# Kernel optimization log

Measured on AMD Instinct MI355X. Metric: run time of the kernel, lower is better.

## Reference

```python
import jax, jax.numpy as jnp
import numpy as np

B, T, D = 16, 2048, 384
BLOCK = 3
NB = D // BLOCK
EPS = 1e-8


def setup_inputs() -> dict:
    key = jax.random.key(0)
    ks = jax.random.split(key, 8)
    std = 0.02
    quat_sequence = jax.random.normal(ks[0], (B, T, 4), dtype=jnp.float32)
    # weights stored as (in, out); x @ W
    W_in = jax.random.normal(ks[1], (4, D), dtype=jnp.float32) * std
    W_biv = jax.random.normal(ks[2], (D, NB * 3), dtype=jnp.float32) * (1.0 / np.sqrt(D))
    b_biv = jnp.zeros((NB * 3,), dtype=jnp.float32)
    W_dec = jax.random.normal(ks[3], (D, D), dtype=jnp.float32) * (1.0 / np.sqrt(D))
    b_dec = jnp.full((D,), 1.4, dtype=jnp.float32)
    W_inj = jax.random.normal(ks[4], (D, D), dtype=jnp.float32) * (1.0 / np.sqrt(D))
    b_inj = jax.random.normal(ks[5], (D,), dtype=jnp.float32) * (1.0 / np.sqrt(D))
    W_out = jax.random.normal(ks[6], (D, 4), dtype=jnp.float32) * std
    return {
        'quat_sequence': quat_sequence,
        'W_in': W_in, 'W_biv': W_biv, 'b_biv': b_biv,
        'W_dec': W_dec, 'b_dec': b_dec, 'W_inj': W_inj, 'b_inj': b_inj,
        'W_out': W_out,
    }


def _quat_rotate_blocks(h_blocks, bivectors):
    # h_blocks, bivectors: (..., NB, 3)
    norm_b = jnp.clip(jnp.linalg.norm(bivectors, axis=-1, keepdims=True), EPS, None)
    half = norm_b / 2
    w = jnp.cos(half)[..., 0]
    s = (jnp.sin(half) / norm_b)[..., 0]
    qx = s * bivectors[..., 2]
    qy = -s * bivectors[..., 1]
    qz = s * bivectors[..., 0]
    vx, vy, vz = h_blocks[..., 0], h_blocks[..., 1], h_blocks[..., 2]
    tx = 2 * (qy * vz - qz * vy)
    ty = 2 * (qz * vx - qx * vz)
    tz = 2 * (qx * vy - qy * vx)
    rx = vx + w * tx + (qy * tz - qz * ty)
    ry = vy + w * ty + (qz * tx - qx * tz)
    rz = vz + w * tz + (qx * ty - qy * tx)
    return jnp.stack([rx, ry, rz], axis=-1)


def reference(quat_sequence, W_in, W_biv, b_biv, W_dec, b_dec, W_inj, b_inj, W_out):
    hidden_input = quat_sequence @ W_in                       # (B,T,D)
    bivectors_all = (hidden_input @ W_biv + b_biv).reshape(B, T, NB, 3)
    decay_all = jax.nn.sigmoid(hidden_input @ W_dec + b_dec)  # (B,T,D)
    injection_all = hidden_input @ W_inj + b_inj              # (B,T,D)

    def step(h, xs):
        biv, dec, inj = xs  # (B,NB,3), (B,D), (B,D)
        rot = _quat_rotate_blocks(h.reshape(B, NB, 3), biv).reshape(B, D)
        h_next = dec * rot + inj
        return h_next, h_next

    h0 = jnp.zeros((B, D), dtype=quat_sequence.dtype)
    xs = (jnp.swapaxes(bivectors_all, 0, 1),
          jnp.swapaxes(decay_all, 0, 1),
          jnp.swapaxes(injection_all, 0, 1))
    _, hidden_seq = jax.lax.scan(step, h0, xs)                # (T,B,D)
    hidden_output = jnp.swapaxes(hidden_seq, 0, 1)            # (B,T,D)

    predicted_raw = hidden_output @ W_out                     # (B,T,4)
    norm = jnp.clip(jnp.linalg.norm(predicted_raw, axis=-1, keepdims=True), EPS, None)
    return predicted_raw / norm
```

## Files before the change

kernel.cpp:

```cpp
#include <hip/hip_runtime.h>
#include <hip/hip_bf16.h>

#define BB 16
#define TT 2048
#define DD 384
#define GG 2048
#define CC 256
#define LL 8
#define HSTRIDE (DD + 8)
#define EPSF 1e-8f
#define RCPF(x) __builtin_amdgcn_rcpf(x)

__global__ __launch_bounds__(256) void precompute_wc(
        const float* __restrict__ W_in,
        const float* __restrict__ W_biv,
        const float* __restrict__ W_dec,
        const float* __restrict__ W_inj,
        float* __restrict__ Wc) {
    int m = blockIdx.x;
    int jl = threadIdx.x & 15;
    int dp = threadIdx.x >> 4;
    int j = blockIdx.y * 16 + jl;
    const float* __restrict__ W = (m == 0) ? W_biv : (m == 1) ? W_dec : W_inj;
    float a[4] = {0.f, 0.f, 0.f, 0.f};
    for (int d = dp; d < DD; d += 16) {
        float wv = W[d * DD + j];
#pragma unroll
        for (int k = 0; k < 4; ++k) a[k] = fmaf(W_in[k * DD + d], wv, a[k]);
    }
    __shared__ float red[16][17][4];
#pragma unroll
    for (int k = 0; k < 4; ++k) red[dp][jl][k] = a[k];
    __syncthreads();
    for (int s = 8; s >= 1; s >>= 1) {
        if (dp < s) {
#pragma unroll
            for (int k = 0; k < 4; ++k) red[dp][jl][k] += red[dp + s][jl][k];
        }
        __syncthreads();
    }
    if (dp < 4)
        Wc[(size_t)m * 4 * DD + dp * DD + j] = red[0][jl][dp];
}

struct Wts {
    float wb[4][3], wd[4][3], wi[4][3];
    float bb[3], bd[3], bj[3];
};

__device__ __forceinline__ void load_wts(const float* __restrict__ Wc,
                                         const float* __restrict__ b_biv,
                                         const float* __restrict__ b_dec,
                                         const float* __restrict__ b_inj,
                                         int j0, Wts& W) {
    const float* __restrict__ Wb = Wc;
    const float* __restrict__ Wd = Wc + 4 * DD;
    const float* __restrict__ Wi = Wc + 8 * DD;
#pragma unroll
    for (int k = 0; k < 4; ++k)
#pragma unroll
        for (int c = 0; c < 3; ++c) {
            W.wb[k][c] = Wb[k * DD + j0 + c];
            W.wd[k][c] = Wd[k * DD + j0 + c];
            W.wi[k][c] = Wi[k * DD + j0 + c];
        }
#pragma unroll
    for (int c = 0; c < 3; ++c) {
        W.bb[c] = b_biv[j0 + c];
        W.bd[c] = b_dec[j0 + c];
        W.bj[c] = b_inj[j0 + c];
    }
}

#define DOTW(M, c, bias) \
    fmaf(q.w, W.M[3][c], fmaf(q.z, W.M[2][c], fmaf(q.y, W.M[1][c], fmaf(q.x, W.M[0][c], bias))))

__device__ __forceinline__ void step_parts(const Wts& W, float4 q,
        float& dec0, float& dec1, float& dec2,
        float& w, float& qx, float& qy, float& qz,
        float& i0, float& i1, float& i2) {
    float bx = DOTW(wb, 0, W.bb[0]);
    float by = DOTW(wb, 1, W.bb[1]);
    float bz = DOTW(wb, 2, W.bb[2]);
    float d0 = DOTW(wd, 0, W.bd[0]);
    float d1 = DOTW(wd, 1, W.bd[1]);
    float d2 = DOTW(wd, 2, W.bd[2]);
    i0 = DOTW(wi, 0, W.bj[0]);
    i1 = DOTW(wi, 1, W.bj[1]);
    i2 = DOTW(wi, 2, W.bj[2]);
    dec0 = RCPF(1.f + __expf(-d0));
    dec1 = RCPF(1.f + __expf(-d1));
    dec2 = RCPF(1.f + __expf(-d2));
    float u = fmaf(bx, bx, fmaf(by, by, bz * bz));
    w = fmaf(u, fmaf(u, 2.6041667e-3f, -0.125f), 1.f);
    float s = fmaf(u, fmaf(u, 2.6041667e-4f, -2.0833333e-2f), 0.5f);
    qx = s * bz; qy = -s * by; qz = s * bx;
}

__device__ __forceinline__ void step_compose12(const Wts& W, float4 q, float A[12]) {
    float dec0, dec1, dec2, w, qx, qy, qz, i0, i1, i2;
    step_parts(W, q, dec0, dec1, dec2, w, qx, qy, qz, i0, i1, i2);
    float xx = qx*qx, yy = qy*qy, zz = qz*qz;
    float xy = qx*qy, xz = qx*qz, yz = qy*qz;
    float wxs = w*qx, wys = w*qy, wzs = w*qz;
    float M0 = dec0 * (1.f - 2.f*(yy+zz));
    float M1 = dec0 * (2.f*(xy - wzs));
    float M2 = dec0 * (2.f*(xz + wys));
    float M3 = dec1 * (2.f*(xy + wzs));
    float M4 = dec1 * (1.f - 2.f*(xx+zz));
    float M5 = dec1 * (2.f*(yz - wxs));
    float M6 = dec2 * (2.f*(xz - wys));
    float M7 = dec2 * (2.f*(yz + wxs));
    float M8 = dec2 * (1.f - 2.f*(xx+yy));
    float n0 = fmaf(M0, A[0], fmaf(M1, A[3], M2 * A[6]));
    float n1 = fmaf(M0, A[1], fmaf(M1, A[4], M2 * A[7]));
    float n2 = fmaf(M0, A[2], fmaf(M1, A[5], M2 * A[8]));
    float n3 = fmaf(M3, A[0], fmaf(M4, A[3], M5 * A[6]));
    float n4 = fmaf(M3, A[1], fmaf(M4, A[4], M5 * A[7]));
    float n5 = fmaf(M3, A[2], fmaf(M4, A[5], M5 * A[8]));
    float n6 = fmaf(M6, A[0], fmaf(M7, A[3], M8 * A[6]));
    float n7 = fmaf(M6, A[1], fmaf(M7, A[4], M8 * A[7]));
    float n8 = fmaf(M6, A[2], fmaf(M7, A[5], M8 * A[8]));
    float n9  = fmaf(M0, A[9], fmaf(M1, A[10], fmaf(M2, A[11], i0)));
    float n10 = fmaf(M3, A[9], fmaf(M4, A[10], fmaf(M5, A[11], i1)));
    float n11 = fmaf(M6, A[9], fmaf(M7, A[10], fmaf(M8, A[11], i2)));
    A[0]=n0; A[1]=n1; A[2]=n2; A[3]=n3; A[4]=n4; A[5]=n5;
    A[6]=n6; A[7]=n7; A[8]=n8; A[9]=n9; A[10]=n10; A[11]=n11;
}

__device__ __forceinline__ void step_apply(const Wts& W, float4 q,
                                           float& vx, float& vy, float& vz) {
    float dec0, dec1, dec2, w, qx, qy, qz, i0, i1, i2;
    step_parts(W, q, dec0, dec1, dec2, w, qx, qy, qz, i0, i1, i2);
    float tx = 2.f * (qy * vz - qz * vy);
    float ty = 2.f * (qz * vx - qx * vz);
    float tz = 2.f * (qx * vy - qy * vx);
    float rx = vx + w * tx + (qy * tz - qz * ty);
    float ry = vy + w * ty + (qz * tx - qx * tz);
    float rz = vz + w * tz + (qx * ty - qy * tx);
    vx = fmaf(dec0, rx, i0);
    vy = fmaf(dec1, ry, i1);
    vz = fmaf(dec2, rz, i2);
}

#define COMPOSE(R, C, P)                                                    \
    R[0] = fmaf(C[0], P[0], fmaf(C[1], P[3], C[2] * P[6]));                 \
    R[1] = fmaf(C[0], P[1], fmaf(C[1], P[4], C[2] * P[7]));                 \
    R[2] = fmaf(C[0], P[2], fmaf(C[1], P[5], C[2] * P[8]));                 \
    R[3] = fmaf(C[3], P[0], fmaf(C[4], P[3], C[5] * P[6]));                 \
    R[4] = fmaf(C[3], P[1], fmaf(C[4], P[4], C[5] * P[7]));                 \
    R[5] = fmaf(C[3], P[2], fmaf(C[4], P[5], C[5] * P[8]));                 \
    R[6] = fmaf(C[6], P[0], fmaf(C[7], P[3], C[8] * P[6]));                 \
    R[7] = fmaf(C[6], P[1], fmaf(C[7], P[4], C[8] * P[7]));                 \
    R[8] = fmaf(C[6], P[2], fmaf(C[7], P[5], C[8] * P[8]));                 \
    R[9]  = fmaf(C[0], P[9], fmaf(C[1], P[10], fmaf(C[2], P[11], C[9])));   \
    R[10] = fmaf(C[3], P[9], fmaf(C[4], P[10], fmaf(C[5], P[11], C[10])));  \
    R[11] = fmaf(C[6], P[9], fmaf(C[7], P[10], fmaf(C[8], P[11], C[11])));

__global__ __launch_bounds__(128) void chunk_compose(
        const float* __restrict__ quat,
        const float* __restrict__ Wc,
        const float* __restrict__ b_biv,
        const float* __restrict__ b_dec,
        const float* __restrict__ b_inj,
        float* __restrict__ Aff) {
    int c = blockIdx.x, b = blockIdx.y, n = threadIdx.x;
    int g = b * 128 + n, j0 = 3 * n;

    const float4* __restrict__ qp = (const float4*)(quat + (size_t)b * TT * 4) + c * LL;
    float4 q[LL];
#pragma unroll
    for (int t = 0; t < LL; ++t) q[t] = qp[t];

    Wts W;
    load_wts(Wc, b_biv, b_dec, b_inj, j0, W);

    float A[12] = {1.f,0.f,0.f, 0.f,1.f,0.f, 0.f,0.f,1.f, 0.f,0.f,0.f};
#pragma unroll
    for (int t = 0; t < LL; ++t) step_compose12(W, q[t], A);

    float4* o = (float4*)(Aff + ((size_t)c * GG + g) * 12);
    o[0] = make_float4(A[0], A[1], A[2], A[3]);
    o[1] = make_float4(A[4], A[5], A[6], A[7]);
    o[2] = make_float4(A[8], A[9], A[10], A[11]);
}

__global__ __launch_bounds__(256) void chunk_scan(
        const float* __restrict__ Aff,
        float4* __restrict__ Hs) {
    int g = (blockIdx.x * 256 + threadIdx.x) >> 6;
    int l = threadIdx.x & 63;

    float m[4][12];
#pragma unroll
    for (int k = 0; k < 4; ++k) {
        const float4* a = (const float4*)(Aff + ((size_t)(4 * l + k) * GG + g) * 12);
        float4 a0 = a[0], a1 = a[1], a2 = a[2];
        m[k][0]=a0.x; m[k][1]=a0.y; m[k][2]=a0.z; m[k][3]=a0.w;
        m[k][4]=a1.x; m[k][5]=a1.y; m[k][6]=a1.z; m[k][7]=a1.w;
        m[k][8]=a2.x; m[k][9]=a2.y; m[k][10]=a2.z; m[k][11]=a2.w;
    }
    float q01[12], q012[12], Q[12];
    COMPOSE(q01, m[1], m[0]);
    COMPOSE(q012, m[2], q01);
    COMPOSE(Q, m[3], q012);

    float P[12];
#pragma unroll
    for (int k = 0; k < 12; ++k) P[k] = __shfl_up(Q[k], 1);
    if (l == 0) {
        P[0]=1.f; P[1]=0.f; P[2]=0.f; P[3]=0.f; P[4]=1.f; P[5]=0.f;
        P[6]=0.f; P[7]=0.f; P[8]=1.f; P[9]=0.f; P[10]=0.f; P[11]=0.f;
    }
#pragma unroll
    for (int sft = 1; sft < 64; sft <<= 1) {
        float S[12], N[12];
#pragma unroll
        for (int k = 0; k < 12; ++k) S[k] = __shfl_up(P[k], sft);
        COMPOSE(N, P, S);
        bool act = (l >= sft);
#pragma unroll
        for (int k = 0; k < 12; ++k) P[k] = act ? N[k] : P[k];
    }

    float h0 = P[9], h1 = P[10], h2 = P[11];
#pragma unroll
    for (int k = 0; k < 4; ++k) {
        Hs[(size_t)(4 * l + k) * GG + g] = make_float4(h0, h1, h2, 0.f);
        if (k < 3) {
            float n0 = fmaf(m[k][0], h0, fmaf(m[k][1], h1, fmaf(m[k][2], h2, m[k][9])));
            float n1 = fmaf(m[k][3], h0, fmaf(m[k][4], h1, fmaf(m[k][5], h2, m[k][10])));
            float n2 = fmaf(m[k][6], h0, fmaf(m[k][7], h1, fmaf(m[k][8], h2, m[k][11])));
            h0 = n0; h1 = n1; h2 = n2;
        }
    }
}

__global__ __launch_bounds__(128) void chunk_apply_out(
        const float* __restrict__ quat,
        const float* __restrict__ Wc,
        const float* __restrict__ b_biv,
        const float* __restrict__ b_dec,
        const float* __restrict__ b_inj,
        const float* __restrict__ W_out,
        const float4* __restrict__ Hs,
        float* __restrict__ out) {
    int c = blockIdx.x, b = blockIdx.y, n = threadIdx.x;
    int g = b * 128 + n, j0 = 3 * n;

    const float4* __restrict__ qp = (const float4*)(quat + (size_t)b * TT * 4) + c * LL;
    float4 q[LL];
#pragma unroll
    for (int t = 0; t < LL; ++t) q[t] = qp[t];

    float4 h4 = Hs[(size_t)c * GG + g];

    Wts W;
    load_wts(Wc, b_biv, b_dec, b_inj, j0, W);

    __shared__ float H[LL][HSTRIDE];

    float vx = h4.x, vy = h4.y, vz = h4.z;
#pragma unroll
    for (int t = 0; t < LL; ++t) {
        step_apply(W, q[t], vx, vy, vz);
        H[t][j0] = vx; H[t][j0 + 1] = vy; H[t][j0 + 2] = vz;
    }
    __syncthreads();

    int r = n >> 4, p = n & 15;
    float s0 = 0.f, s1 = 0.f, s2 = 0.f, s3 = 0.f;
#pragma unroll 8
    for (int j = 0; j < DD / 16; ++j) {
        int d = p + 16 * j;
        float hv = H[r][d];
        float4 wv = *(const float4*)(W_out + (size_t)d * 4);
        s0 = fmaf(hv, wv.x, s0);
        s1 = fmaf(hv, wv.y, s1);
        s2 = fmaf(hv, wv.z, s2);
        s3 = fmaf(hv, wv.w, s3);
    }
#pragma unroll
    for (int off = 1; off <= 8; off <<= 1) {
        s0 += __shfl_xor(s0, off);
        s1 += __shfl_xor(s1, off);
        s2 += __shfl_xor(s2, off);
        s3 += __shfl_xor(s3, off);
    }
    if (p == 0) {
        float norm = fmaxf(sqrtf(fmaf(s0, s0, fmaf(s1, s1, fmaf(s2, s2, s3 * s3)))), EPSF);
        float inv = RCPF(norm);
        float* outp = out + ((size_t)b * TT + (size_t)c * LL + r) * 4;
        *(float4*)outp = make_float4(s0 * inv, s1 * inv, s2 * inv, s3 * inv);
    }
}

extern "C" void kernel_launch(void* const* d_in, const int* in_sizes, int n_in,
                              void* d_out, int out_size, void* d_ws, size_t ws_size,
                              hipStream_t stream) {
    const float* quat  = (const float*)d_in[0];
    const float* W_in  = (const float*)d_in[1];
    const float* W_biv = (const float*)d_in[2];
    const float* b_biv = (const float*)d_in[3];
    const float* W_dec = (const float*)d_in[4];
    const float* b_dec = (const float*)d_in[5];
    const float* W_inj = (const float*)d_in[6];
    const float* b_inj = (const float*)d_in[7];
    const float* W_out = (const float*)d_in[8];
    float* out = (float*)d_out;

    const size_t AFF_OFF = 32768;
    const size_t AFF_B   = (size_t)CC * GG * 12 * sizeof(float);
    const size_t HS_OFF  = AFF_OFF + AFF_B;

    float*  Wc  = (float*)d_ws;
    float*  Aff = (float*)((char*)d_ws + AFF_OFF);
    float4* Hs  = (float4*)((char*)d_ws + HS_OFF);

    precompute_wc<<<dim3(3, DD / 16), dim3(256), 0, stream>>>(W_in, W_biv, W_dec, W_inj, Wc);
    chunk_compose<<<dim3(CC, BB), dim3(128), 0, stream>>>(quat, Wc, b_biv, b_dec, b_inj, Aff);
    chunk_scan<<<dim3(GG / 4), dim3(256), 0, stream>>>(Aff, Hs);
    chunk_apply_out<<<dim3(CC, BB), dim3(128), 0, stream>>>(quat, Wc, b_biv, b_dec, b_inj,
                                                            W_out, Hs, out);
}
```

Baseline: 63.01 us.

## Store chunk affine maps in fp16 and pack weights as float4

The per-chunk 12-element affine transforms written by chunk_compose and read by chunk_scan are now stored as packed half2 (32 bytes instead of 48), which cuts the intermediate traffic. The folded weights and biases are repacked into a float4-per-neuron layout so load_wts uses vector loads. The first compose step now initializes from the step matrix instead of multiplying by the identity. Storing the transforms in fp16 loses precision in the scanned recurrence, which may hurt accuracy.

```diff
diff --git a/kernel.cpp b/kernel.cpp
--- a/kernel.cpp
+++ b/kernel.cpp
@@ -1,5 +1,6 @@
 #include <hip/hip_runtime.h>
 #include <hip/hip_bf16.h>
+#include <hip/hip_fp16.h>
 
 #define BB 16
 #define TT 2048
@@ -11,11 +12,15 @@
 #define EPSF 1e-8f
 #define RCPF(x) __builtin_amdgcn_rcpf(x)
 
+
 __global__ __launch_bounds__(256) void precompute_wc(
         const float* __restrict__ W_in,
         const float* __restrict__ W_biv,
         const float* __restrict__ W_dec,
         const float* __restrict__ W_inj,
+        const float* __restrict__ b_biv,
+        const float* __restrict__ b_dec,
+        const float* __restrict__ b_inj,
         float* __restrict__ Wc) {
     int m = blockIdx.x;
     int jl = threadIdx.x & 15;
@@ -39,8 +44,17 @@
         }
         __syncthreads();
     }
-    if (dp < 4)
-        Wc[(size_t)m * 4 * DD + dp * DD + j] = red[0][jl][dp];
+    int n = j / 3, comp = j - 3 * n;
+    if (dp < 4) {
+        Wc[((m * 4 + dp) * 128 + n) * 4 + comp] = red[0][jl][dp];
+    } else if (dp == 4) {
+#pragma unroll
+        for (int k = 0; k < 4; ++k) Wc[((m * 4 + k) * 128 + n) * 4 + 3] = 0.f;
+        Wc[(1536 + m * 128 + n) * 4 + 3] = 0.f;
+    } else if (dp == 5) {
+        const float* bsrc = (m == 0) ? b_biv : (m == 1) ? b_dec : b_inj;
+        Wc[(1536 + m * 128 + n) * 4 + comp] = bsrc[j];
+    }
 }
 
 struct Wts {
@@ -48,28 +62,28 @@
     float bb[3], bd[3], bj[3];
 };
 
-__device__ __forceinline__ void load_wts(const float* __restrict__ Wc,
-                                         const float* __restrict__ b_biv,
-                                         const float* __restrict__ b_dec,
-                                         const float* __restrict__ b_inj,
-                                         int j0, Wts& W) {
-    const float* __restrict__ Wb = Wc;
-    const float* __restrict__ Wd = Wc + 4 * DD;
-    const float* __restrict__ Wi = Wc + 8 * DD;
-#pragma unroll
-    for (int k = 0; k < 4; ++k)
-#pragma unroll
-        for (int c = 0; c < 3; ++c) {
-            W.wb[k][c] = Wb[k * DD + j0 + c];
-            W.wd[k][c] = Wd[k * DD + j0 + c];
-            W.wi[k][c] = Wi[k * DD + j0 + c];
-        }
-#pragma unroll
-    for (int c = 0; c < 3; ++c) {
-        W.bb[c] = b_biv[j0 + c];
-        W.bd[c] = b_dec[j0 + c];
-        W.bj[c] = b_inj[j0 + c];
-    }
+__device__ __forceinline__ void load_wts(const float4* __restrict__ Wc4, int n, Wts& W) {
+#pragma unroll
+    for (int k = 0; k < 4; ++k) {
+        float4 v = Wc4[(0 * 4 + k) * 128 + n];
+        W.wb[k][0] = v.x; W.wb[k][1] = v.y; W.wb[k][2] = v.z;
+    }
+#pragma unroll
+    for (int k = 0; k < 4; ++k) {
+        float4 v = Wc4[(1 * 4 + k) * 128 + n];
+        W.wd[k][0] = v.x; W.wd[k][1] = v.y; W.wd[k][2] = v.z;
+    }
+#pragma unroll
+    for (int k = 0; k < 4; ++k) {
+        float4 v = Wc4[(2 * 4 + k) * 128 + n];
+        W.wi[k][0] = v.x; W.wi[k][1] = v.y; W.wi[k][2] = v.z;
+    }
+    float4 b0 = Wc4[1536 + 0 * 128 + n];
+    float4 b1 = Wc4[1536 + 1 * 128 + n];
+    float4 b2 = Wc4[1536 + 2 * 128 + n];
+    W.bb[0] = b0.x; W.bb[1] = b0.y; W.bb[2] = b0.z;
+    W.bd[0] = b1.x; W.bd[1] = b1.y; W.bd[2] = b1.z;
+    W.bj[0] = b2.x; W.bj[1] = b2.y; W.bj[2] = b2.z;
 }
 
 #define DOTW(M, c, bias) \
@@ -97,33 +111,47 @@
     qx = s * bz; qy = -s * by; qz = s * bx;
 }
 
-__device__ __forceinline__ void step_compose12(const Wts& W, float4 q, float A[12]) {
-    float dec0, dec1, dec2, w, qx, qy, qz, i0, i1, i2;
+__device__ __forceinline__ void step_matrix(const Wts& W, float4 q,
+                                            float M[9], float& i0, float& i1, float& i2) {
+    float dec0, dec1, dec2, w, qx, qy, qz;
     step_parts(W, q, dec0, dec1, dec2, w, qx, qy, qz, i0, i1, i2);
     float xx = qx*qx, yy = qy*qy, zz = qz*qz;
     float xy = qx*qy, xz = qx*qz, yz = qy*qz;
     float wxs = w*qx, wys = w*qy, wzs = w*qz;
-    float M0 = dec0 * (1.f - 2.f*(yy+zz));
-    float M1 = dec0 * (2.f*(xy - wzs));
-    float M2 = dec0 * (2.f*(xz + wys));
-    float M3 = dec1 * (2.f*(xy + wzs));
-    float M4 = dec1 * (1.f - 2.f*(xx+zz));
-    float M5 = dec1 * (2.f*(yz - wxs));
-    float M6 = dec2 * (2.f*(xz - wys));
-    float M7 = dec2 * (2.f*(yz + wxs));
-    float M8 = dec2 * (1.f - 2.f*(xx+yy));
-    float n0 = fmaf(M0, A[0], fmaf(M1, A[3], M2 * A[6]));
-    float n1 = fmaf(M0, A[1], fmaf(M1, A[4], M2 * A[7]));
-    float n2 = fmaf(M0, A[2], fmaf(M1, A[5], M2 * A[8]));
-    float n3 = fmaf(M3, A[0], fmaf(M4, A[3], M5 * A[6]));
-    float n4 = fmaf(M3, A[1], fmaf(M4, A[4], M5 * A[7]));
-    float n5 = fmaf(M3, A[2], fmaf(M4, A[5], M5 * A[8]));
-    float n6 = fmaf(M6, A[0], fmaf(M7, A[3], M8 * A[6]));
-    float n7 = fmaf(M6, A[1], fmaf(M7, A[4], M8 * A[7]));
-    float n8 = fmaf(M6, A[2], fmaf(M7, A[5], M8 * A[8]));
-    float n9  = fmaf(M0, A[9], fmaf(M1, A[10], fmaf(M2, A[11], i0)));
-    float n10 = fmaf(M3, A[9], fmaf(M4, A[10], fmaf(M5, A[11], i1)));
-    float n11 = fmaf(M6, A[9], fmaf(M7, A[10], fmaf(M8, A[11], i2)));
+    M[0] = dec0 * (1.f - 2.f*(yy+zz));
+    M[1] = dec0 * (2.f*(xy - wzs));
+    M[2] = dec0 * (2.f*(xz + wys));
+    M[3] = dec1 * (2.f*(xy + wzs));
+    M[4] = dec1 * (1.f - 2.f*(xx+zz));
+    M[5] = dec1 * (2.f*(yz - wxs));
+    M[6] = dec2 * (2.f*(xz - wys));
+    M[7] = dec2 * (2.f*(yz + wxs));
+    M[8] = dec2 * (1.f - 2.f*(xx+yy));
+}
+
+__device__ __forceinline__ void step_init12(const Wts& W, float4 q, float A[12]) {
+    float M[9], i0, i1, i2;
+    step_matrix(W, q, M, i0, i1, i2);
+#pragma unroll
+    for (int e = 0; e < 9; ++e) A[e] = M[e];
+    A[9] = i0; A[10] = i1; A[11] = i2;
+}
+
+__device__ __forceinline__ void step_compose12(const Wts& W, float4 q, float A[12]) {
+    float M[9], i0, i1, i2;
+    step_matrix(W, q, M, i0, i1, i2);
+    float n0 = fmaf(M[0], A[0], fmaf(M[1], A[3], M[2] * A[6]));
+    float n1 = fmaf(M[0], A[1], fmaf(M[1], A[4], M[2] * A[7]));
+    float n2 = fmaf(M[0], A[2], fmaf(M[1], A[5], M[2] * A[8]));
+    float n3 = fmaf(M[3], A[0], fmaf(M[4], A[3], M[5] * A[6]));
+    float n4 = fmaf(M[3], A[1], fmaf(M[4], A[4], M[5] * A[7]));
+    float n5 = fmaf(M[3], A[2], fmaf(M[4], A[5], M[5] * A[8]));
+    float n6 = fmaf(M[6], A[0], fmaf(M[7], A[3], M[8] * A[6]));
+    float n7 = fmaf(M[6], A[1], fmaf(M[7], A[4], M[8] * A[7]));
+    float n8 = fmaf(M[6], A[2], fmaf(M[7], A[5], M[8] * A[8]));
+    float n9  = fmaf(M[0], A[9], fmaf(M[1], A[10], fmaf(M[2], A[11], i0)));
+    float n10 = fmaf(M[3], A[9], fmaf(M[4], A[10], fmaf(M[5], A[11], i1)));
+    float n11 = fmaf(M[6], A[9], fmaf(M[7], A[10], fmaf(M[8], A[11], i2)));
     A[0]=n0; A[1]=n1; A[2]=n2; A[3]=n3; A[4]=n4; A[5]=n5;
     A[6]=n6; A[7]=n7; A[8]=n8; A[9]=n9; A[10]=n10; A[11]=n11;
 }
@@ -159,13 +187,10 @@
 
 __global__ __launch_bounds__(128) void chunk_compose(
         const float* __restrict__ quat,
-        const float* __restrict__ Wc,
-        const float* __restrict__ b_biv,
-        const float* __restrict__ b_dec,
-        const float* __restrict__ b_inj,
-        float* __restrict__ Aff) {
+        const float4* __restrict__ Wc4,
+        float4* __restrict__ AffH) {
     int c = blockIdx.x, b = blockIdx.y, n = threadIdx.x;
-    int g = b * 128 + n, j0 = 3 * n;
+    int g = b * 128 + n;
 
     const float4* __restrict__ qp = (const float4*)(quat + (size_t)b * TT * 4) + c * LL;
     float4 q[LL];
@@ -173,20 +198,25 @@
     for (int t = 0; t < LL; ++t) q[t] = qp[t];
 
     Wts W;
-    load_wts(Wc, b_biv, b_dec, b_inj, j0, W);
-
-    float A[12] = {1.f,0.f,0.f, 0.f,1.f,0.f, 0.f,0.f,1.f, 0.f,0.f,0.f};
-#pragma unroll
-    for (int t = 0; t < LL; ++t) step_compose12(W, q[t], A);
-
-    float4* o = (float4*)(Aff + ((size_t)c * GG + g) * 12);
-    o[0] = make_float4(A[0], A[1], A[2], A[3]);
-    o[1] = make_float4(A[4], A[5], A[6], A[7]);
-    o[2] = make_float4(A[8], A[9], A[10], A[11]);
+    load_wts(Wc4, n, W);
+
+    float A[12];
+    step_init12(W, q[0], A);
+#pragma unroll
+    for (int t = 1; t < LL; ++t) step_compose12(W, q[t], A);
+
+    union { __half2 h2[8]; float4 f4[2]; } u;
+#pragma unroll
+    for (int e = 0; e < 6; ++e) u.h2[e] = __floats2half2_rn(A[2 * e], A[2 * e + 1]);
+    u.h2[6] = __floats2half2_rn(0.f, 0.f);
+    u.h2[7] = __floats2half2_rn(0.f, 0.f);
+    float4* o = AffH + ((size_t)c * GG + g) * 2;
+    o[0] = u.f4[0];
+    o[1] = u.f4[1];
 }
 
 __global__ __launch_bounds__(256) void chunk_scan(
-        const float* __restrict__ Aff,
+        const float4* __restrict__ AffH,
         float4* __restrict__ Hs) {
     int g = (blockIdx.x * 256 + threadIdx.x) >> 6;
     int l = threadIdx.x & 63;
@@ -194,11 +224,14 @@
     float m[4][12];
 #pragma unroll
     for (int k = 0; k < 4; ++k) {
-        const float4* a = (const float4*)(Aff + ((size_t)(4 * l + k) * GG + g) * 12);
-        float4 a0 = a[0], a1 = a[1], a2 = a[2];
-        m[k][0]=a0.x; m[k][1]=a0.y; m[k][2]=a0.z; m[k][3]=a0.w;
-        m[k][4]=a1.x; m[k][5]=a1.y; m[k][6]=a1.z; m[k][7]=a1.w;
-        m[k][8]=a2.x; m[k][9]=a2.y; m[k][10]=a2.z; m[k][11]=a2.w;
+        const float4* a = AffH + ((size_t)(4 * l + k) * GG + g) * 2;
+        union { __half2 h2[8]; float4 f4[2]; } u;
+        u.f4[0] = a[0]; u.f4[1] = a[1];
+#pragma unroll
+        for (int e = 0; e < 6; ++e) {
+            float2 v = __half22float2(u.h2[e]);
+            m[k][2 * e] = v.x; m[k][2 * e + 1] = v.y;
+        }
     }
     float q01[12], q012[12], Q[12];
     COMPOSE(q01, m[1], m[0]);
@@ -238,15 +271,12 @@
 
 __global__ __launch_bounds__(128) void chunk_apply_out(
         const float* __restrict__ quat,
-        const float* __restrict__ Wc,
-        const float* __restrict__ b_biv,
-        const float* __restrict__ b_dec,
-        const float* __restrict__ b_inj,
+        const float4* __restrict__ Wc4,
         const float* __restrict__ W_out,
         const float4* __restrict__ Hs,
         float* __restrict__ out) {
     int c = blockIdx.x, b = blockIdx.y, n = threadIdx.x;
-    int g = b * 128 + n, j0 = 3 * n;
+    int g = b * 128 + n;
 
     const float4* __restrict__ qp = (const float4*)(quat + (size_t)b * TT * 4) + c * LL;
     float4 q[LL];
@@ -256,10 +286,11 @@
     float4 h4 = Hs[(size_t)c * GG + g];
 
     Wts W;
-    load_wts(Wc, b_biv, b_dec, b_inj, j0, W);
+    load_wts(Wc4, n, W);
 
     __shared__ float H[LL][HSTRIDE];
 
+    int j0 = 3 * n;
     float vx = h4.x, vy = h4.y, vz = h4.z;
 #pragma unroll
     for (int t = 0; t < LL; ++t) {
@@ -310,16 +341,17 @@
     float* out = (float*)d_out;
 
     const size_t AFF_OFF = 32768;
-    const size_t AFF_B   = (size_t)CC * GG * 12 * sizeof(float);
+    const size_t AFF_B   = (size_t)CC * GG * 32;
     const size_t HS_OFF  = AFF_OFF + AFF_B;
 
-    float*  Wc  = (float*)d_ws;
-    float*  Aff = (float*)((char*)d_ws + AFF_OFF);
-    float4* Hs  = (float4*)((char*)d_ws + HS_OFF);
-
-    precompute_wc<<<dim3(3, DD / 16), dim3(256), 0, stream>>>(W_in, W_biv, W_dec, W_inj, Wc);
-    chunk_compose<<<dim3(CC, BB), dim3(128), 0, stream>>>(quat, Wc, b_biv, b_dec, b_inj, Aff);
-    chunk_scan<<<dim3(GG / 4), dim3(256), 0, stream>>>(Aff, Hs);
-    chunk_apply_out<<<dim3(CC, BB), dim3(128), 0, stream>>>(quat, Wc, b_biv, b_dec, b_inj,
-                                                            W_out, Hs, out);
-}
+    float*  Wc   = (float*)d_ws;
+    float4* Wc4  = (float4*)d_ws;
+    float4* AffH = (float4*)((char*)d_ws + AFF_OFF);
+    float4* Hs   = (float4*)((char*)d_ws + HS_OFF);
+
+    precompute_wc<<<dim3(3, DD / 16), dim3(256), 0, stream>>>(
+        W_in, W_biv, W_dec, W_inj, b_biv, b_dec, b_inj, Wc);
+    chunk_compose<<<dim3(CC, BB), dim3(128), 0, stream>>>(quat, Wc4, AffH);
+    chunk_scan<<<dim3(GG / 4), dim3(256), 0, stream>>>(AffH, Hs);
+    chunk_apply_out<<<dim3(CC, BB), dim3(128), 0, stream>>>(quat, Wc4, W_out, Hs, out);
+}
```

Measured after the change: 59.83 us. -5.0%, faster.
